# Kernel optimization log

Measured on AMD Instinct MI355X. Metric: run time of the kernel, lower is better.

## Reference

```python
import jax, jax.numpy as jnp
import numpy as np


def setup_inputs() -> dict:
    key = jax.random.key(0)
    k1, k2 = jax.random.split(key)
    B, C, H, W = 64, 512, 28, 28
    x = jax.random.normal(k1, (B, C, H, W), dtype=jnp.float32)
    cc = jax.random.randint(k2, (B, H, W), 0, 2).astype(jnp.bool_)
    return {"x": x, "cc": cc}


def reference(x, cc):
    # x: [B, C, H, W], cc: [B, H, W] bool mask
    m = cc.astype(x.dtype)
    # ave_pool: tmp initialized to x[:, :, 0, 0], then accumulates masked positions
    masked_sum = jnp.einsum('bchw,bhw->bc', x, m) + x[:, :, 0, 0]  # [B, C]
    cnt = jnp.sum(m, axis=(1, 2))                                   # [B]
    denom = jnp.where(cnt == 0, jnp.ones_like(cnt), cnt)            # count==0 -> no division
    mean_pool = masked_sum / denom[:, None]                         # [B, C]
    # AdaptiveMaxPool2d(1): global spatial max
    max_pool = jnp.max(x, axis=(2, 3))                              # [B, C]
    return jnp.concatenate([mean_pool, max_pool], axis=1)           # [B, 2C]
```

## Files before the change

kernel.cpp:

```cpp
#include <hip/hip_runtime.h>


#define HW 784
#define NC 512
#define NB 64

__global__ __launch_bounds__(256) void pool_model_kernel(
    const float* __restrict__ x,
    const void* __restrict__ cc,
    float* __restrict__ out)
{
    __shared__ float sm[HW];
    __shared__ float s_cnt;
    __shared__ int s_bad_int;
    __shared__ int s_bad_flt;

    const int b     = blockIdx.x >> 7;
    const int chunk = blockIdx.x & 127;
    const int t     = threadIdx.x;

    if (t == 0) { s_bad_int = 0; s_bad_flt = 0; s_cnt = 0.0f; }
    __syncthreads();

    const int* cci = (const int*)cc;
    if (t < 196) {
        int v = cci[b * 196 + t];
        if (v & ~1) atomicOr(&s_bad_int, 1);
        if (v != 0 && v != 0x3F800000) atomicOr(&s_bad_flt, 1);
    }
    __syncthreads();

    float local = 0.0f;
    if (s_bad_int == 0) {
        const int* row = cci + (size_t)b * HW;
        for (int i = t; i < HW; i += 256) {
            float mv = (float)row[i];
            sm[i] = mv; local += mv;
        }
    } else if (s_bad_flt == 0) {
        const float* row = (const float*)cc + (size_t)b * HW;
        for (int i = t; i < HW; i += 256) {
            float mv = row[i];
            sm[i] = mv; local += mv;
        }
    } else {
        const unsigned char* row = (const unsigned char*)cc + (size_t)b * HW;
        for (int i = t; i < HW; i += 256) {
            float mv = (float)row[i];
            sm[i] = mv; local += mv;
        }
    }
    atomicAdd(&s_cnt, local);
    __syncthreads();

    const float cnt   = s_cnt;
    const float denom = (cnt == 0.0f) ? 1.0f : cnt;

    const int wave = t >> 6;
    const int lane = t & 63;
    const int c    = chunk * 4 + wave;

    const float4* xr = (const float4*)(x + (size_t)(b * NC + c) * HW);
    float sum = 0.0f;
    float mx  = -INFINITY;
    for (int v = lane; v < 196; v += 64) {
        float4 q  = xr[v];
        float4 m4 = *(const float4*)(sm + v * 4);
        sum += q.x * m4.x + q.y * m4.y + q.z * m4.z + q.w * m4.w;
        mx = fmaxf(mx, fmaxf(fmaxf(q.x, q.y), fmaxf(q.z, q.w)));
        if (v == 0) sum += q.x;
    }
    for (int off = 32; off > 0; off >>= 1) {
        sum += __shfl_down(sum, off);
        mx  = fmaxf(mx, __shfl_down(mx, off));
    }
    if (lane == 0) {
        out[(size_t)b * (2 * NC) + c]      = sum / denom;
        out[(size_t)b * (2 * NC) + NC + c] = mx;
    }
}

extern "C" void kernel_launch(void* const* d_in, const int* in_sizes, int n_in,
                              void* d_out, int out_size, void* d_ws, size_t ws_size,
                              hipStream_t stream) {
    const float* x  = (const float*)d_in[0];
    const void*  cc = d_in[1];
    float* out = (float*)d_out;
    pool_model_kernel<<<dim3(NB * 128), dim3(256), 0, stream>>>(x, cc, out);
}
```

Measured before the change: 165.7 us.

## Split mask preparation into a separate kernel and process four channels per wave

Moves mask decoding and count computation into a small prep kernel that writes a float mask and inverse denominator to workspace. The main kernel loads the mask once into registers per wave and processes four channels per wave with fully unrolled float4 loads, cutting grid size by four and removing per-block mask decoding and shared-memory syncs. It replaces the division with a multiply by a precomputed reciprocal. The cost is an extra kernel launch and a global round-trip for the mask.

```diff
diff --git a/kernel.cpp b/kernel.cpp
--- a/kernel.cpp
+++ b/kernel.cpp
@@ -1,30 +1,25 @@
 #include <hip/hip_runtime.h>
 
 
-#define HW 784
-#define NC 512
-#define NB 64
+#define HW   784
+#define NV4  196
+#define NC   512
+#define NB   64
 
-__global__ __launch_bounds__(256) void pool_model_kernel(
-    const float* __restrict__ x,
-    const void* __restrict__ cc,
-    float* __restrict__ out)
+__global__ __launch_bounds__(256) void mask_prep_kernel(
+    const void* __restrict__ cc, float* __restrict__ mask_f,
+    float* __restrict__ invd)
 {
-    __shared__ float sm[HW];
     __shared__ float s_cnt;
-    __shared__ int s_bad_int;
-    __shared__ int s_bad_flt;
-
-    const int b     = blockIdx.x >> 7;
-    const int chunk = blockIdx.x & 127;
-    const int t     = threadIdx.x;
-
-    if (t == 0) { s_bad_int = 0; s_bad_flt = 0; s_cnt = 0.0f; }
+    __shared__ int s_bad_int, s_bad_flt;
+    const int b = blockIdx.x;
+    const int t = threadIdx.x;
+    if (t == 0) { s_cnt = 0.0f; s_bad_int = 0; s_bad_flt = 0; }
     __syncthreads();
 
     const int* cci = (const int*)cc;
-    if (t < 196) {
-        int v = cci[b * 196 + t];
+    if (t < NV4) {
+        int v = cci[b * NV4 + t];
         if (v & ~1) atomicOr(&s_bad_int, 1);
         if (v != 0 && v != 0x3F800000) atomicOr(&s_bad_flt, 1);
     }
@@ -35,48 +30,85 @@
         const int* row = cci + (size_t)b * HW;
         for (int i = t; i < HW; i += 256) {
             float mv = (float)row[i];
-            sm[i] = mv; local += mv;
+            mask_f[b * HW + i] = mv; local += mv;
         }
     } else if (s_bad_flt == 0) {
         const float* row = (const float*)cc + (size_t)b * HW;
         for (int i = t; i < HW; i += 256) {
             float mv = row[i];
-            sm[i] = mv; local += mv;
+            mask_f[b * HW + i] = mv; local += mv;
         }
     } else {
         const unsigned char* row = (const unsigned char*)cc + (size_t)b * HW;
         for (int i = t; i < HW; i += 256) {
             float mv = (float)row[i];
-            sm[i] = mv; local += mv;
+            mask_f[b * HW + i] = mv; local += mv;
         }
     }
     atomicAdd(&s_cnt, local);
     __syncthreads();
+    if (t == 0) {
+        float c = s_cnt;
+        invd[b] = 1.0f / ((c == 0.0f) ? 1.0f : c);
+    }
+}
 
-    const float cnt   = s_cnt;
-    const float denom = (cnt == 0.0f) ? 1.0f : cnt;
+__device__ __forceinline__ float dot4(float4 a, float4 b) {
+    return a.x * b.x + a.y * b.y + a.z * b.z + a.w * b.w;
+}
+__device__ __forceinline__ float max4(float4 a) {
+    return fmaxf(fmaxf(a.x, a.y), fmaxf(a.z, a.w));
+}
 
+__global__ __launch_bounds__(256) void pool_main_kernel(
+    const float* __restrict__ x, const float* __restrict__ mask_f,
+    const float* __restrict__ invd, float* __restrict__ out)
+{
+    const int blk  = blockIdx.x;
+    const int b    = blk >> 5;
+    const int grp  = blk & 31;
+    const int t    = threadIdx.x;
     const int wave = t >> 6;
     const int lane = t & 63;
-    const int c    = chunk * 4 + wave;
+    const int c0   = grp * 16 + wave * 4;
 
-    const float4* xr = (const float4*)(x + (size_t)(b * NC + c) * HW);
-    float sum = 0.0f;
-    float mx  = -INFINITY;
-    for (int v = lane; v < 196; v += 64) {
-        float4 q  = xr[v];
-        float4 m4 = *(const float4*)(sm + v * 4);
-        sum += q.x * m4.x + q.y * m4.y + q.z * m4.z + q.w * m4.w;
-        mx = fmaxf(mx, fmaxf(fmaxf(q.x, q.y), fmaxf(q.z, q.w)));
-        if (v == 0) sum += q.x;
+    const float4* m4 = (const float4*)(mask_f + (size_t)b * HW);
+    float4 m0 = m4[lane];
+    float4 m1 = m4[lane + 64];
+    float4 m2 = m4[lane + 128];
+    float4 m3 = (lane < 4) ? m4[lane + 192] : make_float4(0.f, 0.f, 0.f, 0.f);
+    const float inv = invd[b];
+
+    float s[4], mx[4];
+#pragma unroll
+    for (int j = 0; j < 4; ++j) {
+        const float4* xr = (const float4*)(x + (size_t)(b * NC + c0 + j) * HW);
+        float4 q0 = xr[lane];
+        float4 q1 = xr[lane + 64];
+        float4 q2 = xr[lane + 128];
+        float sum = dot4(q0, m0) + dot4(q1, m1) + dot4(q2, m2);
+        float mm  = fmaxf(fmaxf(max4(q0), max4(q1)), max4(q2));
+        if (lane < 4) {
+            float4 q3 = xr[lane + 192];
+            sum += dot4(q3, m3);
+            mm = fmaxf(mm, max4(q3));
+        }
+        if (lane == 0) sum += q0.x;
+        s[j] = sum; mx[j] = mm;
     }
-    for (int off = 32; off > 0; off >>= 1) {
-        sum += __shfl_down(sum, off);
-        mx  = fmaxf(mx, __shfl_down(mx, off));
-    }
-    if (lane == 0) {
-        out[(size_t)b * (2 * NC) + c]      = sum / denom;
-        out[(size_t)b * (2 * NC) + NC + c] = mx;
+
+#pragma unroll
+    for (int j = 0; j < 4; ++j) {
+        float sum = s[j], mm = mx[j];
+        for (int off = 32; off > 0; off >>= 1) {
+            sum += __shfl_down(sum, off);
+            mm   = fmaxf(mm, __shfl_down(mm, off));
+        }
+        if (lane == 0) {
+            const int c = c0 + j;
+            out[(size_t)b * (2 * NC) + c]      = sum * inv;
+            out[(size_t)b * (2 * NC) + NC + c] = mm;
+        }
     }
 }
 
@@ -85,6 +117,10 @@
                               hipStream_t stream) {
     const float* x  = (const float*)d_in[0];
     const void*  cc = d_in[1];
-    float* out = (float*)d_out;
-    pool_model_kernel<<<dim3(NB * 128), dim3(256), 0, stream>>>(x, cc, out);
+    float* out    = (float*)d_out;
+    float* mask_f = (float*)d_ws;
+    float* invd   = (float*)d_ws + (size_t)NB * HW;
+
+    mask_prep_kernel<<<dim3(NB), dim3(256), 0, stream>>>(cc, mask_f, invd);
+    pool_main_kernel<<<dim3(NB * 32), dim3(256), 0, stream>>>(x, mask_f, invd, out);
 }
```

Result: faster. 155.6 us (-6.1%).
